# Kernel tuning notes

Measured on AMD Instinct MI355X. Metric: run time of the kernel, lower is better.

Reference implementation:

```python
import jax, jax.numpy as jnp
import numpy as np

B, I, H = 8192, 1024, 1024

def setup_inputs() -> dict:
    key = jax.random.key(0)
    ks = jax.random.split(key, 5)
    return {
        "x": jax.random.normal(ks[0], (B, I), dtype=jnp.float32),
        "m_prev": jax.random.normal(ks[1], (B, H), dtype=jnp.float32),
        "c_prev": jax.random.normal(ks[2], (B, H), dtype=jnp.float32),
        "w_m": jax.random.normal(ks[3], (H, 8 * H), dtype=jnp.float32),
        "w_inputs": jax.random.normal(ks[4], (I, 8 * H), dtype=jnp.float32),
    }

def reference(x, m_prev, c_prev, w_m, w_inputs):
    hidden = w_m.shape[0]
    m_mat = m_prev @ w_m              # [B, 8H]
    in_mat = x @ w_inputs             # [B, 8H]
    # 8-way split along feature dim
    ms = jnp.split(m_mat, 8, axis=1)
    xs = jnp.split(in_mat, 8, axis=1)
    sig, th, rl = jax.nn.sigmoid, jnp.tanh, jax.nn.relu
    l1_0 = sig(xs[0] + ms[0])
    l1_1 = rl(xs[1] + ms[1])
    l1_2 = sig(xs[2] + ms[2])
    l1_3 = rl(xs[3] * ms[3])
    l1_4 = th(xs[4] + ms[4])
    l1_5 = sig(xs[5] + ms[5])
    l1_6 = th(xs[6] + ms[6])
    l1_7 = sig(xs[7] + ms[7])
    l2_0 = th(l1_0 * l1_1)
    l2_1 = th(l1_2 + l1_3)
    l2_2 = th(l1_4 * l1_5)
    l2_3 = sig(l1_6 + l1_7)
    l2_0 = th(l2_0 + c_prev)
    new_c = l2_0 * l2_1
    l3_1 = th(l2_2 + l2_3)
    new_m = th(new_c * l3_1)
    return (new_m, new_c)
```

## Files before the change

### kernel.cpp

```cpp
#include <hip/hip_runtime.h>
#include <stdint.h>
#include <stddef.h>


typedef _Float16 half8 __attribute__((ext_vector_type(8)));
typedef float f32x4 __attribute__((ext_vector_type(4)));
typedef float float4v __attribute__((ext_vector_type(4)));
typedef unsigned int u32;
typedef u32 u32x4 __attribute__((ext_vector_type(4)));

__device__ __forceinline__ float fsig(float x) { return 1.0f / (1.0f + __expf(-x)); }
__device__ __forceinline__ float ftanh(float x) { return 2.0f * fsig(2.0f * x) - 1.0f; }
__device__ __forceinline__ u32 packh(_Float16 a, _Float16 b) {
  union { u32 u; _Float16 h[2]; } p;
  p.h[0] = a; p.h[1] = b; return p.u;
}

__global__ __launch_bounds__(256) void prep_b(
    const float* __restrict__ w_inputs, const float* __restrict__ w_m,
    char* __restrict__ wsB) {
  const int kt = blockIdx.x;
  const int hblk = blockIdx.y;
  const int tid = threadIdx.x;
  const int n = tid & 15;
  const int g = (tid >> 4) & 7;
  const int mat = tid >> 7;
  const float* w = mat ? w_m : w_inputs;
  const float* src = w + (size_t)kt * 32 * 8192 + (size_t)g * 1024 + hblk * 16 + n;
  _Float16 hs[32], ls[32];
#pragma unroll
  for (int k = 0; k < 32; ++k) {
    const float v = src[(size_t)k * 8192];
    const _Float16 h = (_Float16)v;
    hs[k] = h;
    ls[k] = (_Float16)(v - (float)h);
  }
  char* tile = wsB + ((size_t)hblk * 32 + kt) * 32768;
  char* hi = tile + (size_t)((mat * 8 + g) * 2 + 0) * 1024;
  char* lo = hi + 1024;
#pragma unroll
  for (int kc = 0; kc < 4; ++kc) {
    u32x4 a = {packh(hs[kc * 8 + 0], hs[kc * 8 + 1]), packh(hs[kc * 8 + 2], hs[kc * 8 + 3]),
               packh(hs[kc * 8 + 4], hs[kc * 8 + 5]), packh(hs[kc * 8 + 6], hs[kc * 8 + 7])};
    *(u32x4*)(hi + (kc * 16 + n) * 16) = a;
    u32x4 b = {packh(ls[kc * 8 + 0], ls[kc * 8 + 1]), packh(ls[kc * 8 + 2], ls[kc * 8 + 3]),
               packh(ls[kc * 8 + 4], ls[kc * 8 + 5]), packh(ls[kc * 8 + 6], ls[kc * 8 + 7])};
    *(u32x4*)(lo + (kc * 16 + n) * 16) = b;
  }
}

__global__ __launch_bounds__(256) void split_ab(
    const float4v* __restrict__ xin, const float4v* __restrict__ min,
    half8* __restrict__ xhi, half8* __restrict__ xlo,
    half8* __restrict__ mhi, half8* __restrict__ mlo) {
  const int which = blockIdx.y;
  const float4v* in = which ? min : xin;
  half8* hi = which ? mhi : xhi;
  half8* lo = which ? mlo : xlo;
  const size_t idx = (size_t)blockIdx.x * 256 + threadIdx.x;
  const float4v a = in[idx * 2];
  const float4v b = in[idx * 2 + 1];
  half8 h, l;
#pragma unroll
  for (int j = 0; j < 4; ++j) {
    const float v = a[j]; const _Float16 hv = (_Float16)v;
    h[j] = hv; l[j] = (_Float16)(v - (float)hv);
  }
#pragma unroll
  for (int j = 0; j < 4; ++j) {
    const float v = b[j]; const _Float16 hv = (_Float16)v;
    h[4 + j] = hv; l[4 + j] = (_Float16)(v - (float)hv);
  }
  hi[idx] = h; lo[idx] = l;
}

__global__ __launch_bounds__(256, 2) void nascell_v3(
    const _Float16* __restrict__ xh_g, const _Float16* __restrict__ xl_g,
    const _Float16* __restrict__ mh_g, const _Float16* __restrict__ ml_g,
    const char* __restrict__ wsB,
    const float* __restrict__ c_prev,
    float* __restrict__ out) {
  const int tid = threadIdx.x;
  const int wid = tid >> 6;
  const int lane = tid & 63;
  const int row0 = blockIdx.y * 256;
  const int hblk = blockIdx.x;
  const int m16 = lane & 15;
  const int q = lane >> 4;

  const size_t arow = (size_t)(row0 + wid * 64 + m16);
  const _Float16* xhb = xh_g + arow * 1024 + q * 8;
  const _Float16* xlb = xl_g + arow * 1024 + q * 8;
  const _Float16* mhb = mh_g + arow * 1024 + q * 8;
  const _Float16* mlb = ml_g + arow * 1024 + q * 8;

  const char* bt = wsB + (size_t)hblk * 32 * 32768 + lane * 16;

  f32x4 acc[4][9];
#pragma unroll
  for (int r = 0; r < 4; ++r)
#pragma unroll
    for (int gg = 0; gg < 9; ++gg) acc[r][gg] = (f32x4)0.0f;

#pragma unroll 1
  for (int kt = 0; kt < 32; ++kt) {
    const char* tb = bt + (size_t)kt * 32768;

    half8 axh[4], axl[4], amh[4], aml[4];
#pragma unroll
    for (int r = 0; r < 4; ++r) {
      axh[r] = *(const half8*)(xhb + (size_t)r * 16384 + kt * 32);
      axl[r] = *(const half8*)(xlb + (size_t)r * 16384 + kt * 32);
      amh[r] = *(const half8*)(mhb + (size_t)r * 16384 + kt * 32);
      aml[r] = *(const half8*)(mlb + (size_t)r * 16384 + kt * 32);
    }

#pragma unroll
    for (int c = 0; c < 8; ++c) {
      const half8 bxh = *(const half8*)(tb + (size_t)(c * 2) * 1024);
      const half8 bxl = *(const half8*)(tb + (size_t)(c * 2 + 1) * 1024);
#pragma unroll
      for (int r = 0; r < 4; ++r) {
        f32x4 t = acc[r][c];
        t = __builtin_amdgcn_mfma_f32_16x16x32_f16(axh[r], bxh, t, 0, 0, 0);
        t = __builtin_amdgcn_mfma_f32_16x16x32_f16(axh[r], bxl, t, 0, 0, 0);
        t = __builtin_amdgcn_mfma_f32_16x16x32_f16(axl[r], bxh, t, 0, 0, 0);
        acc[r][c] = t;
      }
    }

#pragma unroll
    for (int c = 0; c < 8; ++c) {
      const half8 bmh = *(const half8*)(tb + 16384 + (size_t)(c * 2) * 1024);
      const half8 bml = *(const half8*)(tb + 16384 + (size_t)(c * 2 + 1) * 1024);
      const int tgt = (c == 3) ? 8 : c;
#pragma unroll
      for (int r = 0; r < 4; ++r) {
        f32x4 t = acc[r][tgt];
        t = __builtin_amdgcn_mfma_f32_16x16x32_f16(amh[r], bmh, t, 0, 0, 0);
        t = __builtin_amdgcn_mfma_f32_16x16x32_f16(amh[r], bml, t, 0, 0, 0);
        t = __builtin_amdgcn_mfma_f32_16x16x32_f16(aml[r], bmh, t, 0, 0, 0);
        acc[r][tgt] = t;
      }
    }
  }

  float* out_m = out;
  float* out_c = out + (size_t)8192 * 1024;
  const int h = hblk * 16 + m16;
#pragma unroll
  for (int r = 0; r < 4; ++r) {
#pragma unroll
    for (int i = 0; i < 4; ++i) {
      const int grow = row0 + wid * 64 + r * 16 + q * 4 + i;
      const float p0 = acc[r][0][i], p1 = acc[r][1][i], p2 = acc[r][2][i];
      const float x3 = acc[r][3][i], p4 = acc[r][4][i], p5 = acc[r][5][i];
      const float p6 = acc[r][6][i], p7 = acc[r][7][i], m3 = acc[r][8][i];
      const float cp = c_prev[(size_t)grow * 1024 + h];
      float l1_0 = fsig(p0);
      float l1_1 = fmaxf(p1, 0.0f);
      float l1_2 = fsig(p2);
      float l1_3 = fmaxf(x3 * m3, 0.0f);
      float l1_4 = ftanh(p4);
      float l1_5 = fsig(p5);
      float l1_6 = ftanh(p6);
      float l1_7 = fsig(p7);
      float l2_0 = ftanh(l1_0 * l1_1);
      float l2_1 = ftanh(l1_2 + l1_3);
      float l2_2 = ftanh(l1_4 * l1_5);
      float l2_3 = fsig(l1_6 + l1_7);
      float l2_0b = ftanh(l2_0 + cp);
      float nc = l2_0b * l2_1;
      float l3_1 = ftanh(l2_2 + l2_3);
      float nm = ftanh(nc * l3_1);
      out_m[(size_t)grow * 1024 + h] = nm;
      out_c[(size_t)grow * 1024 + h] = nc;
    }
  }
}

__global__ __launch_bounds__(256, 2) void nascell_main(
    const float* __restrict__ x,
    const float* __restrict__ m_prev,
    const float* __restrict__ c_prev,
    const float* __restrict__ w_inputs,
    const float* __restrict__ w_m,
    float* __restrict__ out) {
  __shared__ short lds[17408];
  const int tid = threadIdx.x;
  const int wid = tid >> 6;
  const int lane = tid & 63;
  const int row0 = blockIdx.y * 256;
  const int h0 = blockIdx.x * 16;
  const int m16 = lane & 15;
  const int q = lane >> 4;

  const int bmat = tid >> 7;
  const int bg = (tid >> 4) & 7;
  const int bkp = (tid & 15) * 2;
  const float* wsrc = bmat ? w_m : w_inputs;
  const float* wrow_base = wsrc + (size_t)bkp * 8192 + (size_t)bg * 1024 + (size_t)h0;
  short* bh = lds + bmat * 4352 + bg * 544 + (bkp ^ ((bg & 3) << 3));
  short* bl = bh + 8704;

  const float* axp[4];
  const float* amp[4];
#pragma unroll
  for (int r = 0; r < 4; ++r) {
    const size_t arow = (size_t)(row0 + wid * 64 + r * 16 + m16);
    axp[r] = x + arow * 1024 + q * 8;
    amp[r] = m_prev + arow * 1024 + q * 8;
  }

  f32x4 acc[4][9];
#pragma unroll
  for (int r = 0; r < 4; ++r)
#pragma unroll
    for (int gg = 0; gg < 9; ++gg) acc[r][gg] = (f32x4)0.0f;

  for (int kt = 0; kt < 32; ++kt) {
    const float* wr = wrow_base + (size_t)kt * 32 * 8192;
    float4v b0 = *(const float4v*)(wr);
    float4v b1 = *(const float4v*)(wr + 4);
    float4v b2 = *(const float4v*)(wr + 8);
    float4v b3 = *(const float4v*)(wr + 12);
    float4v d0 = *(const float4v*)(wr + 8192);
    float4v d1 = *(const float4v*)(wr + 8196);
    float4v d2 = *(const float4v*)(wr + 8200);
    float4v d3 = *(const float4v*)(wr + 8204);

    float4v xa[4][2];
#pragma unroll
    for (int r = 0; r < 4; ++r) {
      xa[r][0] = *(const float4v*)(axp[r] + kt * 32);
      xa[r][1] = *(const float4v*)(axp[r] + kt * 32 + 4);
    }

    __syncthreads();

#pragma unroll
    for (int n = 0; n < 16; ++n) {
      const float r0 = (n < 4 ? b0[n & 3] : n < 8 ? b1[n & 3] : n < 12 ? b2[n & 3] : b3[n & 3]);
      const float r1 = (n < 4 ? d0[n & 3] : n < 8 ? d1[n & 3] : n < 12 ? d2[n & 3] : d3[n & 3]);
      const _Float16 h0v = (_Float16)r0;
      const _Float16 h1v = (_Float16)r1;
      *(u32*)(bh + n * 32) = packh(h0v, h1v);
      const _Float16 l0v = (_Float16)(r0 - (float)h0v);
      const _Float16 l1v = (_Float16)(r1 - (float)h1v);
      *(u32*)(bl + n * 32) = packh(l0v, l1v);
    }

    half8 axh[4], axl[4];
#pragma unroll
    for (int r = 0; r < 4; ++r)
#pragma unroll
      for (int j = 0; j < 8; ++j) {
        const float v = xa[r][j >> 2][j & 3];
        const _Float16 hv = (_Float16)v;
        axh[r][j] = hv;
        axl[r][j] = (_Float16)(v - (float)hv);
      }

    __syncthreads();

    float4v ma[4][2];
#pragma unroll
    for (int r = 0; r < 4; ++r) {
      ma[r][0] = *(const float4v*)(amp[r] + kt * 32);
      ma[r][1] = *(const float4v*)(amp[r] + kt * 32 + 4);
    }

#pragma unroll
    for (int c = 0; c < 8; ++c) {
      const int qs = (q ^ (c & 3)) * 8;
      const int bo = c * 544 + m16 * 32 + qs;
      half8 bxh = *(const half8*)(lds + bo);
      half8 bxl = *(const half8*)(lds + 8704 + bo);
#pragma unroll
      for (int r = 0; r < 4; ++r) {
        f32x4 t = acc[r][c];
        t = __builtin_amdgcn_mfma_f32_16x16x32_f16(axh[r], bxh, t, 0, 0, 0);
        t = __builtin_amdgcn_mfma_f32_16x16x32_f16(axh[r], bxl, t, 0, 0, 0);
        t = __builtin_amdgcn_mfma_f32_16x16x32_f16(axl[r], bxh, t, 0, 0, 0);
        acc[r][c] = t;
      }
    }

    half8 amh[4], aml[4];
#pragma unroll
    for (int r = 0; r < 4; ++r)
#pragma unroll
      for (int j = 0; j < 8; ++j) {
        const float v = ma[r][j >> 2][j & 3];
        const _Float16 hv = (_Float16)v;
        amh[r][j] = hv;
        aml[r][j] = (_Float16)(v - (float)hv);
      }

#pragma unroll
    for (int c = 0; c < 8; ++c) {
      const int qs = (q ^ (c & 3)) * 8;
      const int bo = 4352 + c * 544 + m16 * 32 + qs;
      half8 bmh = *(const half8*)(lds + bo);
      half8 bml = *(const half8*)(lds + 8704 + bo);
      const int tgt = (c == 3) ? 8 : c;
#pragma unroll
      for (int r = 0; r < 4; ++r) {
        f32x4 t = acc[r][tgt];
        t = __builtin_amdgcn_mfma_f32_16x16x32_f16(amh[r], bmh, t, 0, 0, 0);
        t = __builtin_amdgcn_mfma_f32_16x16x32_f16(amh[r], bml, t, 0, 0, 0);
        t = __builtin_amdgcn_mfma_f32_16x16x32_f16(aml[r], bmh, t, 0, 0, 0);
        acc[r][tgt] = t;
      }
    }
  }

  float* out_m = out;
  float* out_c = out + (size_t)8192 * 1024;
  const int h = h0 + m16;
#pragma unroll
  for (int r = 0; r < 4; ++r) {
#pragma unroll
    for (int i = 0; i < 4; ++i) {
      const int grow = row0 + wid * 64 + r * 16 + q * 4 + i;
      const float p0 = acc[r][0][i], p1 = acc[r][1][i], p2 = acc[r][2][i];
      const float x3 = acc[r][3][i], p4 = acc[r][4][i], p5 = acc[r][5][i];
      const float p6 = acc[r][6][i], p7 = acc[r][7][i], m3 = acc[r][8][i];
      const float cp = c_prev[(size_t)grow * 1024 + h];
      float l1_0 = fsig(p0);
      float l1_1 = fmaxf(p1, 0.0f);
      float l1_2 = fsig(p2);
      float l1_3 = fmaxf(x3 * m3, 0.0f);
      float l1_4 = ftanh(p4);
      float l1_5 = fsig(p5);
      float l1_6 = ftanh(p6);
      float l1_7 = fsig(p7);
      float l2_0 = ftanh(l1_0 * l1_1);
      float l2_1 = ftanh(l1_2 + l1_3);
      float l2_2 = ftanh(l1_4 * l1_5);
      float l2_3 = fsig(l1_6 + l1_7);
      float l2_0b = ftanh(l2_0 + cp);
      float nc = l2_0b * l2_1;
      float l3_1 = ftanh(l2_2 + l2_3);
      float nm = ftanh(nc * l3_1);
      out_m[(size_t)grow * 1024 + h] = nm;
      out_c[(size_t)grow * 1024 + h] = nc;
    }
  }
}

extern "C" void kernel_launch(void* const* d_in, const int* in_sizes, int n_in,
                              void* d_out, int out_size, void* d_ws, size_t ws_size,
                              hipStream_t stream) {
  (void)in_sizes; (void)n_in; (void)out_size;
  const float* x        = (const float*)d_in[0];
  const float* m_prev   = (const float*)d_in[1];
  const float* c_prev   = (const float*)d_in[2];
  const float* w_m      = (const float*)d_in[3];
  const float* w_inputs = (const float*)d_in[4];
  float* out = (float*)d_out;

  if (ws_size >= 134217728ull && d_ws != nullptr) {
    char* wsB = (char*)d_ws;
    _Float16* xh = (_Float16*)((char*)d_ws + 67108864);
    _Float16* xl = xh + 8388608;
    _Float16* mh = xl + 8388608;
    _Float16* ml = mh + 8388608;
    prep_b<<<dim3(32, 64), 256, 0, stream>>>(w_inputs, w_m, wsB);
    split_ab<<<dim3(4096, 2), 256, 0, stream>>>(
        (const float4v*)x, (const float4v*)m_prev,
        (half8*)xh, (half8*)xl, (half8*)mh, (half8*)ml);
    nascell_v3<<<dim3(64, 32), 256, 0, stream>>>(xh, xl, mh, ml, wsB, c_prev, out);
  } else {
    dim3 grid(64, 32);
    nascell_main<<<grid, 256, 0, stream>>>(x, m_prev, c_prev, w_inputs, w_m, out);
  }
}
```

Before: 1.053 ms.

## Switch main GEMM to 32x32 MFMA with double-buffered LDS weight staging

```diff
diff --git a/kernel.cpp b/kernel.cpp
--- a/kernel.cpp
+++ b/kernel.cpp
@@ -4,16 +4,23 @@
 
 
 typedef _Float16 half8 __attribute__((ext_vector_type(8)));
-typedef float f32x4 __attribute__((ext_vector_type(4)));
+typedef float f32x16 __attribute__((ext_vector_type(16)));
 typedef float float4v __attribute__((ext_vector_type(4)));
 typedef unsigned int u32;
 typedef u32 u32x4 __attribute__((ext_vector_type(4)));
+typedef float f32x4 __attribute__((ext_vector_type(4)));
 
 __device__ __forceinline__ float fsig(float x) { return 1.0f / (1.0f + __expf(-x)); }
 __device__ __forceinline__ float ftanh(float x) { return 2.0f * fsig(2.0f * x) - 1.0f; }
 __device__ __forceinline__ u32 packh(_Float16 a, _Float16 b) {
   union { u32 u; _Float16 h[2]; } p;
   p.h[0] = a; p.h[1] = b; return p.u;
+}
+
+__device__ __forceinline__ void gload16(const void* g, void* l) {
+  __builtin_amdgcn_global_load_lds(
+      (const __attribute__((address_space(1))) void*)g,
+      (__attribute__((address_space(3))) void*)l, 16, 0, 0);
 }
 
 __global__ __launch_bounds__(256) void prep_b(
@@ -25,6 +32,9 @@
   const int n = tid & 15;
   const int g = (tid >> 4) & 7;
   const int mat = tid >> 7;
+  const int pr = g >> 1;
+  const int hsel = g & 1;
+  const int c = hsel * 16 + n;
   const float* w = mat ? w_m : w_inputs;
   const float* src = w + (size_t)kt * 32 * 8192 + (size_t)g * 1024 + hblk * 16 + n;
   _Float16 hs[32], ls[32];
@@ -36,16 +46,19 @@
     ls[k] = (_Float16)(v - (float)h);
   }
   char* tile = wsB + ((size_t)hblk * 32 + kt) * 32768;
-  char* hi = tile + (size_t)((mat * 8 + g) * 2 + 0) * 1024;
-  char* lo = hi + 1024;
-#pragma unroll
-  for (int kc = 0; kc < 4; ++kc) {
-    u32x4 a = {packh(hs[kc * 8 + 0], hs[kc * 8 + 1]), packh(hs[kc * 8 + 2], hs[kc * 8 + 3]),
-               packh(hs[kc * 8 + 4], hs[kc * 8 + 5]), packh(hs[kc * 8 + 6], hs[kc * 8 + 7])};
-    *(u32x4*)(hi + (kc * 16 + n) * 16) = a;
-    u32x4 b = {packh(ls[kc * 8 + 0], ls[kc * 8 + 1]), packh(ls[kc * 8 + 2], ls[kc * 8 + 3]),
-               packh(ls[kc * 8 + 4], ls[kc * 8 + 5]), packh(ls[kc * 8 + 6], ls[kc * 8 + 7])};
-    *(u32x4*)(lo + (kc * 16 + n) * 16) = b;
+#pragma unroll
+  for (int ks = 0; ks < 2; ++ks) {
+#pragma unroll
+    for (int lh = 0; lh < 2; ++lh) {
+      const int lane = lh * 32 + c;
+      const int kb = ks * 16 + lh * 8;
+      u32x4 H = {packh(hs[kb + 0], hs[kb + 1]), packh(hs[kb + 2], hs[kb + 3]),
+                 packh(hs[kb + 4], hs[kb + 5]), packh(hs[kb + 6], hs[kb + 7])};
+      *(u32x4*)(tile + (size_t)((((mat * 4 + pr) * 2 + ks) * 2 + 0) * 1024 + lane * 16)) = H;
+      u32x4 L = {packh(ls[kb + 0], ls[kb + 1]), packh(ls[kb + 2], ls[kb + 3]),
+                 packh(ls[kb + 4], ls[kb + 5]), packh(ls[kb + 6], ls[kb + 7])};
+      *(u32x4*)(tile + (size_t)((((mat * 4 + pr) * 2 + ks) * 2 + 1) * 1024 + lane * 16)) = L;
+    }
   }
 }
 
@@ -74,27 +87,186 @@
   hi[idx] = h; lo[idx] = l;
 }
 
-__global__ __launch_bounds__(256, 2) void nascell_v3(
+__global__ __launch_bounds__(256, 2) void nascell_v4(
     const _Float16* __restrict__ xh_g, const _Float16* __restrict__ xl_g,
     const _Float16* __restrict__ mh_g, const _Float16* __restrict__ ml_g,
     const char* __restrict__ wsB,
     const float* __restrict__ c_prev,
     float* __restrict__ out) {
+  __shared__ char lds[65536];
   const int tid = threadIdx.x;
   const int wid = tid >> 6;
   const int lane = tid & 63;
   const int row0 = blockIdx.y * 256;
   const int hblk = blockIdx.x;
+  const int l31 = lane & 31;
+  const int lh = lane >> 5;
+  const int c16 = lane & 15;
+  const int hsel = (lane >> 4) & 1;
+
+  const _Float16* xhb[2]; const _Float16* xlb[2];
+  const _Float16* mhb[2]; const _Float16* mlb[2];
+#pragma unroll
+  for (int rg = 0; rg < 2; ++rg) {
+    const size_t arow = (size_t)(row0 + wid * 64 + rg * 32 + l31);
+    xhb[rg] = xh_g + arow * 1024 + lh * 8;
+    xlb[rg] = xl_g + arow * 1024 + lh * 8;
+    mhb[rg] = mh_g + arow * 1024 + lh * 8;
+    mlb[rg] = ml_g + arow * 1024 + lh * 8;
+  }
+
+  const char* wsb = wsB + (size_t)hblk * 32 * 32768 + tid * 16;
+  char* ldsme = lds + tid * 16;
+
+  f32x16 aX[2][4];
+  f32x16 aE[2];
+#pragma unroll
+  for (int rg = 0; rg < 2; ++rg) {
+#pragma unroll
+    for (int p = 0; p < 4; ++p) aX[rg][p] = (f32x16)0.0f;
+    aE[rg] = (f32x16)0.0f;
+  }
+
+#pragma unroll
+  for (int r = 0; r < 8; ++r) gload16(wsb + r * 4096, ldsme + r * 4096);
+
+  for (int kt = 0; kt < 32; ++kt) {
+    __syncthreads();
+
+    half8 axh[2][2], axl[2][2], amh[2][2], aml[2][2];
+#pragma unroll
+    for (int rg = 0; rg < 2; ++rg)
+#pragma unroll
+      for (int ks = 0; ks < 2; ++ks) {
+        axh[rg][ks] = *(const half8*)(xhb[rg] + kt * 32 + ks * 16);
+        axl[rg][ks] = *(const half8*)(xlb[rg] + kt * 32 + ks * 16);
+        amh[rg][ks] = *(const half8*)(mhb[rg] + kt * 32 + ks * 16);
+        aml[rg][ks] = *(const half8*)(mlb[rg] + kt * 32 + ks * 16);
+      }
+    __builtin_amdgcn_sched_barrier(0);
+    if (kt < 31) {
+      const char* src = wsb + (size_t)(kt + 1) * 32768;
+      char* dst = lds + ((kt + 1) & 1) * 32768 + tid * 16;
+#pragma unroll
+      for (int r = 0; r < 8; ++r) gload16(src + r * 4096, dst + r * 4096);
+    }
+    __builtin_amdgcn_sched_barrier(0);
+
+    const char* bb = lds + (kt & 1) * 32768 + (size_t)lane * 16;
+
+    __builtin_amdgcn_s_setprio(1);
+#pragma unroll
+    for (int ks = 0; ks < 2; ++ks)
+#pragma unroll
+      for (int pr = 0; pr < 4; ++pr) {
+        const half8 bh = *(const half8*)(bb + (size_t)(((pr * 2 + ks) * 2 + 0) * 1024));
+        const half8 bl = *(const half8*)(bb + (size_t)(((pr * 2 + ks) * 2 + 1) * 1024));
+#pragma unroll
+        for (int rg = 0; rg < 2; ++rg) {
+          f32x16 t = aX[rg][pr];
+          t = __builtin_amdgcn_mfma_f32_32x32x16_f16(axh[rg][ks], bh, t, 0, 0, 0);
+          t = __builtin_amdgcn_mfma_f32_32x32x16_f16(axh[rg][ks], bl, t, 0, 0, 0);
+          t = __builtin_amdgcn_mfma_f32_32x32x16_f16(axl[rg][ks], bh, t, 0, 0, 0);
+          aX[rg][pr] = t;
+        }
+      }
+#pragma unroll
+    for (int ks = 0; ks < 2; ++ks)
+#pragma unroll
+      for (int pr = 0; pr < 4; ++pr) {
+        const half8 bh = *(const half8*)(bb + (size_t)((((4 + pr) * 2 + ks) * 2 + 0) * 1024));
+        const half8 bl = *(const half8*)(bb + (size_t)((((4 + pr) * 2 + ks) * 2 + 1) * 1024));
+#pragma unroll
+        for (int rg = 0; rg < 2; ++rg) {
+          f32x16 t = (pr == 1) ? aE[rg] : aX[rg][pr];
+          t = __builtin_amdgcn_mfma_f32_32x32x16_f16(amh[rg][ks], bh, t, 0, 0, 0);
+          t = __builtin_amdgcn_mfma_f32_32x32x16_f16(amh[rg][ks], bl, t, 0, 0, 0);
+          t = __builtin_amdgcn_mfma_f32_32x32x16_f16(aml[rg][ks], bh, t, 0, 0, 0);
+          if (pr == 1) aE[rg] = t; else aX[rg][pr] = t;
+        }
+      }
+    __builtin_amdgcn_s_setprio(0);
+  }
+
+  float* out_m = out;
+  float* out_c = out + (size_t)8192 * 1024;
+  const int h = hblk * 16 + c16;
+#pragma unroll
+  for (int rg = 0; rg < 2; ++rg) {
+#pragma unroll
+    for (int reg = 0; reg < 16; ++reg) {
+      const float o0 = aX[rg][0][reg], o1 = aX[rg][1][reg];
+      const float o2 = aX[rg][2][reg], o3 = aX[rg][3][reg];
+      const float oE = aE[rg][reg];
+      const float r0 = __shfl_xor(o0, 16, 64);
+      const float r1 = __shfl_xor(o1, 16, 64);
+      const float r2 = __shfl_xor(o2, 16, 64);
+      const float r3 = __shfl_xor(o3, 16, 64);
+      const float rE = __shfl_xor(oE, 16, 64);
+      const bool mine = (reg < 8) ? (hsel == 0) : (hsel == 1);
+      if (mine) {
+        const float p0 = hsel ? r0 : o0, p1 = hsel ? o0 : r0;
+        const float x2 = hsel ? r1 : o1, x3 = hsel ? o1 : r1;
+        const float m2 = hsel ? rE : oE, m3 = hsel ? oE : rE;
+        const float p4 = hsel ? r2 : o2, p5 = hsel ? o2 : r2;
+        const float p6 = hsel ? r3 : o3, p7 = hsel ? o3 : r3;
+        const int grow = row0 + wid * 64 + rg * 32 + (reg & 3) + 8 * (reg >> 2) + 4 * lh;
+        const float cp = c_prev[(size_t)grow * 1024 + h];
+        float l1_0 = fsig(p0);
+        float l1_1 = fmaxf(p1, 0.0f);
+        float l1_2 = fsig(x2 + m2);
+        float l1_3 = fmaxf(x3 * m3, 0.0f);
+        float l1_4 = ftanh(p4);
+        float l1_5 = fsig(p5);
+        float l1_6 = ftanh(p6);
+        float l1_7 = fsig(p7);
+        float l2_0 = ftanh(l1_0 * l1_1);
+        float l2_1 = ftanh(l1_2 + l1_3);
+        float l2_2 = ftanh(l1_4 * l1_5);
+        float l2_3 = fsig(l1_6 + l1_7);
+        float l2_0b = ftanh(l2_0 + cp);
+        float nc = l2_0b * l2_1;
+        float l3_1 = ftanh(l2_2 + l2_3);
+        float nm = ftanh(nc * l3_1);
+        out_m[(size_t)grow * 1024 + h] = nm;
+        out_c[(size_t)grow * 1024 + h] = nc;
+      }
+    }
+  }
+}
+
+__global__ __launch_bounds__(256, 2) void nascell_main(
+    const float* __restrict__ x,
+    const float* __restrict__ m_prev,
+    const float* __restrict__ c_prev,
+    const float* __restrict__ w_inputs,
+    const float* __restrict__ w_m,
+    float* __restrict__ out) {
+  __shared__ short lds[17408];
+  const int tid = threadIdx.x;
+  const int wid = tid >> 6;
+  const int lane = tid & 63;
+  const int row0 = blockIdx.y * 256;
+  const int h0 = blockIdx.x * 16;
   const int m16 = lane & 15;
   const int q = lane >> 4;
 
-  const size_t arow = (size_t)(row0 + wid * 64 + m16);
-  const _Float16* xhb = xh_g + arow * 1024 + q * 8;
-  const _Float16* xlb = xl_g + arow * 1024 + q * 8;
-  const _Float16* mhb = mh_g + arow * 1024 + q * 8;
-  const _Float16* mlb = ml_g + arow * 1024 + q * 8;
-
-  const char* bt = wsB + (size_t)hblk * 32 * 32768 + lane * 16;
+  const int bmat = tid >> 7;
+  const int bg = (tid >> 4) & 7;
+  const int bkp = (tid & 15) * 2;
+  const float* wsrc = bmat ? w_m : w_inputs;
+  const float* wrow_base = wsrc + (size_t)bkp * 8192 + (size_t)bg * 1024 + (size_t)h0;
+  short* bh = lds + bmat * 4352 + bg * 544 + (bkp ^ ((bg & 3) << 3));
+  short* bl = bh + 8704;
+
+  const float* axp[4];
+  const float* amp[4];
+#pragma unroll
+  for (int r = 0; r < 4; ++r) {
+    const size_t arow = (size_t)(row0 + wid * 64 + r * 16 + m16);
+    axp[r] = x + arow * 1024 + q * 8;
+    amp[r] = m_prev + arow * 1024 + q * 8;
+  }
 
   f32x4 acc[4][9];
 #pragma unroll
@@ -102,23 +274,64 @@
 #pragma unroll
     for (int gg = 0; gg < 9; ++gg) acc[r][gg] = (f32x4)0.0f;
 
-#pragma unroll 1
   for (int kt = 0; kt < 32; ++kt) {
-    const char* tb = bt + (size_t)kt * 32768;
-
-    half8 axh[4], axl[4], amh[4], aml[4];
+    const float* wr = wrow_base + (size_t)kt * 32 * 8192;
+    float4v b0 = *(const float4v*)(wr);
+    float4v b1 = *(const float4v*)(wr + 4);
+    float4v b2 = *(const float4v*)(wr + 8);
+    float4v b3 = *(const float4v*)(wr + 12);
+    float4v d0 = *(const float4v*)(wr + 8192);
+    float4v d1 = *(const float4v*)(wr + 8196);
+    float4v d2 = *(const float4v*)(wr + 8200);
+    float4v d3 = *(const float4v*)(wr + 8204);
+
+    float4v xa[4][2];
 #pragma unroll
     for (int r = 0; r < 4; ++r) {
-      axh[r] = *(const half8*)(xhb + (size_t)r * 16384 + kt * 32);
-      axl[r] = *(const half8*)(xlb + (size_t)r * 16384 + kt * 32);
-      amh[r] = *(const half8*)(mhb + (size_t)r * 16384 + kt * 32);
-      aml[r] = *(const half8*)(mlb + (size_t)r * 16384 + kt * 32);
+      xa[r][0] = *(const float4v*)(axp[r] + kt * 32);
+      xa[r][1] = *(const float4v*)(axp[r] + kt * 32 + 4);
+    }
+
+    __syncthreads();
+
+#pragma unroll
+    for (int n = 0; n < 16; ++n) {
+      const float r0 = (n < 4 ? b0[n & 3] : n < 8 ? b1[n & 3] : n < 12 ? b2[n & 3] : b3[n & 3]);
+      const float r1 = (n < 4 ? d0[n & 3] : n < 8 ? d1[n & 3] : n < 12 ? d2[n & 3] : d3[n & 3]);
+      const _Float16 h0v = (_Float16)r0;
+      const _Float16 h1v = (_Float16)r1;
+      *(u32*)(bh + n * 32) = packh(h0v, h1v);
+      const _Float16 l0v = (_Float16)(r0 - (float)h0v);
+      const _Float16 l1v = (_Float16)(r1 - (float)h1v);
+      *(u32*)(bl + n * 32) = packh(l0v, l1v);
+    }
+
+    half8 axh[4], axl[4];
+#pragma unroll
+    for (int r = 0; r < 4; ++r)
+#pragma unroll
+      for (int j = 0; j < 8; ++j) {
+        const float v = xa[r][j >> 2][j & 3];
+        const _Float16 hv = (_Float16)v;
+        axh[r][j] = hv;
+        axl[r][j] = (_Float16)(v - (float)hv);
+      }
+
+    __syncthreads();
+
+    float4v ma[4][2];
+#pragma unroll
+    for (int r = 0; r < 4; ++r) {
+      ma[r][0] = *(const float4v*)(amp[r] + kt * 32);
+      ma[r][1] = *(const float4v*)(amp[r] + kt * 32 + 4);
     }
 
 #pragma unroll
     for (int c = 0; c < 8; ++c) {
-      const half8 bxh = *(const half8*)(tb + (size_t)(c * 2) * 1024);
-      const half8 bxl = *(const half8*)(tb + (size_t)(c * 2 + 1) * 1024);
+      const int qs = (q ^ (c & 3)) * 8;
+      const int bo = c * 544 + m16 * 32 + qs;
+      half8 bxh = *(const half8*)(lds + bo);
+      half8 bxl = *(const half8*)(lds + 8704 + bo);
 #pragma unroll
       for (int r = 0; r < 4; ++r) {
         f32x4 t = acc[r][c];
@@ -129,10 +342,23 @@
       }
     }
 
+    half8 amh[4], aml[4];
+#pragma unroll
+    for (int r = 0; r < 4; ++r)
+#pragma unroll
+      for (int j = 0; j < 8; ++j) {
+        const float v = ma[r][j >> 2][j & 3];
+        const _Float16 hv = (_Float16)v;
+        amh[r][j] = hv;
+        aml[r][j] = (_Float16)(v - (float)hv);
+      }
+
 #pragma unroll
     for (int c = 0; c < 8; ++c) {
-      const half8 bmh = *(const half8*)(tb + 16384 + (size_t)(c * 2) * 1024);
-      const half8 bml = *(const half8*)(tb + 16384 + (size_t)(c * 2 + 1) * 1024);
+      const int qs = (q ^ (c & 3)) * 8;
+      const int bo = 4352 + c * 544 + m16 * 32 + qs;
+      half8 bmh = *(const half8*)(lds + bo);
+      half8 bml = *(const half8*)(lds + 8704 + bo);
       const int tgt = (c == 3) ? 8 : c;
 #pragma unroll
       for (int r = 0; r < 4; ++r) {
@@ -147,7 +373,7 @@
 
   float* out_m = out;
   float* out_c = out + (size_t)8192 * 1024;
-  const int h = hblk * 16 + m16;
+  const int h = h0 + m16;
 #pragma unroll
   for (int r = 0; r < 4; ++r) {
 #pragma unroll
@@ -179,176 +405,6 @@
   }
 }
 
-__global__ __launch_bounds__(256, 2) void nascell_main(
-    const float* __restrict__ x,
-    const float* __restrict__ m_prev,
-    const float* __restrict__ c_prev,
-    const float* __restrict__ w_inputs,
-    const float* __restrict__ w_m,
-    float* __restrict__ out) {
-  __shared__ short lds[17408];
-  const int tid = threadIdx.x;
-  const int wid = tid >> 6;
-  const int lane = tid & 63;
-  const int row0 = blockIdx.y * 256;
-  const int h0 = blockIdx.x * 16;
-  const int m16 = lane & 15;
-  const int q = lane >> 4;
-
-  const int bmat = tid >> 7;
-  const int bg = (tid >> 4) & 7;
-  const int bkp = (tid & 15) * 2;
-  const float* wsrc = bmat ? w_m : w_inputs;
-  const float* wrow_base = wsrc + (size_t)bkp * 8192 + (size_t)bg * 1024 + (size_t)h0;
-  short* bh = lds + bmat * 4352 + bg * 544 + (bkp ^ ((bg & 3) << 3));
-  short* bl = bh + 8704;
-
-  const float* axp[4];
-  const float* amp[4];
-#pragma unroll
-  for (int r = 0; r < 4; ++r) {
-    const size_t arow = (size_t)(row0 + wid * 64 + r * 16 + m16);
-    axp[r] = x + arow * 1024 + q * 8;
-    amp[r] = m_prev + arow * 1024 + q * 8;
-  }
-
-  f32x4 acc[4][9];
-#pragma unroll
-  for (int r = 0; r < 4; ++r)
-#pragma unroll
-    for (int gg = 0; gg < 9; ++gg) acc[r][gg] = (f32x4)0.0f;
-
-  for (int kt = 0; kt < 32; ++kt) {
-    const float* wr = wrow_base + (size_t)kt * 32 * 8192;
-    float4v b0 = *(const float4v*)(wr);
-    float4v b1 = *(const float4v*)(wr + 4);
-    float4v b2 = *(const float4v*)(wr + 8);
-    float4v b3 = *(const float4v*)(wr + 12);
-    float4v d0 = *(const float4v*)(wr + 8192);
-    float4v d1 = *(const float4v*)(wr + 8196);
-    float4v d2 = *(const float4v*)(wr + 8200);
-    float4v d3 = *(const float4v*)(wr + 8204);
-
-    float4v xa[4][2];
-#pragma unroll
-    for (int r = 0; r < 4; ++r) {
-      xa[r][0] = *(const float4v*)(axp[r] + kt * 32);
-      xa[r][1] = *(const float4v*)(axp[r] + kt * 32 + 4);
-    }
-
-    __syncthreads();
-
-#pragma unroll
-    for (int n = 0; n < 16; ++n) {
-      const float r0 = (n < 4 ? b0[n & 3] : n < 8 ? b1[n & 3] : n < 12 ? b2[n & 3] : b3[n & 3]);
-      const float r1 = (n < 4 ? d0[n & 3] : n < 8 ? d1[n & 3] : n < 12 ? d2[n & 3] : d3[n & 3]);
-      const _Float16 h0v = (_Float16)r0;
-      const _Float16 h1v = (_Float16)r1;
-      *(u32*)(bh + n * 32) = packh(h0v, h1v);
-      const _Float16 l0v = (_Float16)(r0 - (float)h0v);
-      const _Float16 l1v = (_Float16)(r1 - (float)h1v);
-      *(u32*)(bl + n * 32) = packh(l0v, l1v);
-    }
-
-    half8 axh[4], axl[4];
-#pragma unroll
-    for (int r = 0; r < 4; ++r)
-#pragma unroll
-      for (int j = 0; j < 8; ++j) {
-        const float v = xa[r][j >> 2][j & 3];
-        const _Float16 hv = (_Float16)v;
-        axh[r][j] = hv;
-        axl[r][j] = (_Float16)(v - (float)hv);
-      }
-
-    __syncthreads();
-
-    float4v ma[4][2];
-#pragma unroll
-    for (int r = 0; r < 4; ++r) {
-      ma[r][0] = *(const float4v*)(amp[r] + kt * 32);
-      ma[r][1] = *(const float4v*)(amp[r] + kt * 32 + 4);
-    }
-
-#pragma unroll
-    for (int c = 0; c < 8; ++c) {
-      const int qs = (q ^ (c & 3)) * 8;
-      const int bo = c * 544 + m16 * 32 + qs;
-      half8 bxh = *(const half8*)(lds + bo);
-      half8 bxl = *(const half8*)(lds + 8704 + bo);
-#pragma unroll
-      for (int r = 0; r < 4; ++r) {
-        f32x4 t = acc[r][c];
-        t = __builtin_amdgcn_mfma_f32_16x16x32_f16(axh[r], bxh, t, 0, 0, 0);
-        t = __builtin_amdgcn_mfma_f32_16x16x32_f16(axh[r], bxl, t, 0, 0, 0);
-        t = __builtin_amdgcn_mfma_f32_16x16x32_f16(axl[r], bxh, t, 0, 0, 0);
-        acc[r][c] = t;
-      }
-    }
-
-    half8 amh[4], aml[4];
-#pragma unroll
-    for (int r = 0; r < 4; ++r)
-#pragma unroll
-      for (int j = 0; j < 8; ++j) {
-        const float v = ma[r][j >> 2][j & 3];
-        const _Float16 hv = (_Float16)v;
-        amh[r][j] = hv;
-        aml[r][j] = (_Float16)(v - (float)hv);
-      }
-
-#pragma unroll
-    for (int c = 0; c < 8; ++c) {
-      const int qs = (q ^ (c & 3)) * 8;
-      const int bo = 4352 + c * 544 + m16 * 32 + qs;
-      half8 bmh = *(const half8*)(lds + bo);
-      half8 bml = *(const half8*)(lds + 8704 + bo);
-      const int tgt = (c == 3) ? 8 : c;
-#pragma unroll
-      for (int r = 0; r < 4; ++r) {
-        f32x4 t = acc[r][tgt];
-        t = __builtin_amdgcn_mfma_f32_16x16x32_f16(amh[r], bmh, t, 0, 0, 0);
-        t = __builtin_amdgcn_mfma_f32_16x16x32_f16(amh[r], bml, t, 0, 0, 0);
-        t = __builtin_amdgcn_mfma_f32_16x16x32_f16(aml[r], bmh, t, 0, 0, 0);
-        acc[r][tgt] = t;
-      }
-    }
-  }
-
-  float* out_m = out;
-  float* out_c = out + (size_t)8192 * 1024;
-  const int h = h0 + m16;
-#pragma unroll
-  for (int r = 0; r < 4; ++r) {
-#pragma unroll
-    for (int i = 0; i < 4; ++i) {
-      const int grow = row0 + wid * 64 + r * 16 + q * 4 + i;
-      const float p0 = acc[r][0][i], p1 = acc[r][1][i], p2 = acc[r][2][i];
-      const float x3 = acc[r][3][i], p4 = acc[r][4][i], p5 = acc[r][5][i];
-      const float p6 = acc[r][6][i], p7 = acc[r][7][i], m3 = acc[r][8][i];
-      const float cp = c_prev[(size_t)grow * 1024 + h];
-      float l1_0 = fsig(p0);
-      float l1_1 = fmaxf(p1, 0.0f);
-      float l1_2 = fsig(p2);
-      float l1_3 = fmaxf(x3 * m3, 0.0f);
-      float l1_4 = ftanh(p4);
-      float l1_5 = fsig(p5);
-      float l1_6 = ftanh(p6);
-      float l1_7 = fsig(p7);
-      float l2_0 = ftanh(l1_0 * l1_1);
-      float l2_1 = ftanh(l1_2 + l1_3);
-      float l2_2 = ftanh(l1_4 * l1_5);
-      float l2_3 = fsig(l1_6 + l1_7);
-      float l2_0b = ftanh(l2_0 + cp);
-      float nc = l2_0b * l2_1;
-      float l3_1 = ftanh(l2_2 + l2_3);
-      float nm = ftanh(nc * l3_1);
-      out_m[(size_t)grow * 1024 + h] = nm;
-      out_c[(size_t)grow * 1024 + h] = nc;
-    }
-  }
-}
-
 extern "C" void kernel_launch(void* const* d_in, const int* in_sizes, int n_in,
                               void* d_out, int out_size, void* d_ws, size_t ws_size,
                               hipStream_t stream) {
@@ -370,7 +426,7 @@
     split_ab<<<dim3(4096, 2), 256, 0, stream>>>(
         (const float4v*)x, (const float4v*)m_prev,
         (half8*)xh, (half8*)xl, (half8*)mh, (half8*)ml);
-    nascell_v3<<<dim3(64, 32), 256, 0, stream>>>(xh, xl, mh, ml, wsB, c_prev, out);
+    nascell_v4<<<dim3(64, 32), 256, 0, stream>>>(xh, xl, mh, ml, wsB, c_prev, out);
   } else {
     dim3 grid(64, 32);
     nascell_main<<<grid, 256, 0, stream>>>(x, m_prev, c_prev, w_inputs, w_m, out);
```

Result: slower. 1.173 ms (+11.4%).
